# Optimization experiments

Hardware: AMD Instinct MI355X
Metric: run time of the kernel (lower is better)

Reference implementation:

```python
import jax, jax.numpy as jnp
import numpy as np

MKT_COEF = jnp.array([0.5, -1.0, 0.8, 0.6, 1.5, 0.4], dtype=jnp.float32)
RISK_COEF = jnp.array([0.5, -0.8, 0.6, 1.0, 1.2, 0.5], dtype=jnp.float32)
PI = 3.14159


def setup_inputs() -> dict:
    key = jax.random.key(0)
    k1, k2, k3, k4 = jax.random.split(key, 4)
    B, S, H, D = 128, 8192, 16, 6
    return {
        "sequence_embeddings": jax.random.normal(k1, (B, S, H), dtype=jnp.float32),
        "market_volatility": jax.random.uniform(k2, (B, S), dtype=jnp.float32),
        "risk_factors": jax.random.normal(k3, (B, S, D), dtype=jnp.float32),
        "router_w": jax.random.normal(k4, (D, H), dtype=jnp.float32) * 0.02,
        "router_b": jnp.zeros((D,), dtype=jnp.float32),
    }


def _expert_predictions(x, assignments):
    # x: (B,S,H); assignments: (B,S) int32
    mean = x.mean(-1, keepdims=True)                       # (B,S,1)
    std = jnp.std(x, axis=-1, keepdims=True, ddof=1)       # torch.std is unbiased
    d0 = jnp.tanh(x[:, :, :4].mean(-1, keepdims=True)) * (1.0 + std)
    d1 = jax.nn.sigmoid(mean) * 0.3 - 0.15
    d2 = x[:, :, :6].mean(-1, keepdims=True) * 0.8 + jnp.sin(x[:, :, 6:10].mean(-1, keepdims=True) * PI) * 0.4
    noise = jax.random.normal(jax.random.key(42), mean.shape, dtype=x.dtype) * 0.05
    d3 = jnp.tanh(x[:, :, :8].mean(-1, keepdims=True)) * 0.9 + noise
    d4 = jax.nn.relu(mean) ** 1.2 + std * 2.5 - 0.5
    d5 = jax.nn.sigmoid(mean) * 0.4 + jnp.tanh(std) * 0.2
    preds_all = jnp.concatenate([d0, d1, d2, d3, d4, d5], axis=-1)  # (B,S,6)
    return jnp.take_along_axis(preds_all, assignments[..., None].astype(jnp.int32), axis=-1)  # (B,S,1)


def reference(sequence_embeddings, market_volatility, risk_factors, router_w, router_b):
    x = sequence_embeddings
    logits = jnp.einsum("bsh,dh->bsd", x, router_w) + router_b            # (B,S,6)
    probs_base = jax.nn.softmax(logits, axis=-1)
    assignments = jnp.argmax(probs_base, axis=-1).astype(jnp.int32)       # (B,S)
    # training-mode market/risk adjusted straight-through probs
    adj = logits + market_volatility[..., None] * MKT_COEF * 0.3 + risk_factors * RISK_COEF * 0.3
    probs_diff = jax.nn.softmax(adj / 1.2, axis=-1)
    routing_probs = jax.lax.stop_gradient(probs_base) + probs_diff - jax.lax.stop_gradient(probs_diff)
    predictions = _expert_predictions(x, assignments)                     # (B,S,1)
    return predictions, routing_probs, assignments
```

## Files before the change

kernel.cpp:

```cpp
#include <hip/hip_runtime.h>
#include <math.h>

typedef float float4v __attribute__((ext_vector_type(4)));
typedef float float2v __attribute__((ext_vector_type(2)));

__device__ __forceinline__ unsigned rotl32(unsigned v, int n) {
  return (v << n) | (v >> (32 - n));
}

__device__ __forceinline__ float frcp(float x) { return __builtin_amdgcn_rcpf(x); }

__device__ __forceinline__ float ftanh(float x) {
  float t = __expf(2.0f * x);
  return 1.0f - 2.0f * frcp(t + 1.0f);
}

__device__ __forceinline__ float fsigmoid(float x) {
  return frcp(1.0f + __expf(-x));
}

__device__ __forceinline__ float jax_threefry_normal42_part(unsigned idx) {
  const unsigned ks0 = 0u;
  const unsigned ks1 = 42u;
  const unsigned ks2 = 0x1BD11BDAu ^ 42u;
  unsigned x0 = 0u + ks0;
  unsigned x1 = idx + ks1;
  const unsigned ks[3] = {ks0, ks1, ks2};
  const int rA[4] = {13, 15, 26, 6};
  const int rB[4] = {17, 29, 16, 24};
#pragma unroll
  for (int i = 0; i < 5; ++i) {
    const int* r = (i & 1) ? rB : rA;
#pragma unroll
    for (int k = 0; k < 4; ++k) {
      x0 += x1;
      x1 = rotl32(x1, r[k]);
      x1 ^= x0;
    }
    x0 += ks[(i + 1) % 3];
    x1 += ks[(i + 2) % 3] + (unsigned)(i + 1);
  }
  unsigned bits = x0 ^ x1;
  float u01 = __uint_as_float((bits >> 9) | 0x3f800000u) - 1.0f;
  const float lo = -0.99999994f;
  float u = fmaxf(lo, fmaf(u01, 2.0f, lo));
  float w = -__logf(1.0f - u * u);
  float p;
  if (w < 5.0f) {
    w = w - 2.5f;
    p = 2.81022636e-08f;
    p = fmaf(p, w, 3.43273939e-07f);
    p = fmaf(p, w, -3.5233877e-06f);
    p = fmaf(p, w, -4.39150654e-06f);
    p = fmaf(p, w, 0.00021858087f);
    p = fmaf(p, w, -0.00125372503f);
    p = fmaf(p, w, -0.00417768164f);
    p = fmaf(p, w, 0.246640727f);
    p = fmaf(p, w, 1.50140941f);
  } else {
    w = sqrtf(w) - 3.0f;
    p = -0.000200214257f;
    p = fmaf(p, w, 0.000100950558f);
    p = fmaf(p, w, 0.00134934322f);
    p = fmaf(p, w, -0.00367342844f);
    p = fmaf(p, w, 0.00573950773f);
    p = fmaf(p, w, -0.0076224613f);
    p = fmaf(p, w, 0.00943887047f);
    p = fmaf(p, w, 1.00167406f);
    p = fmaf(p, w, 2.83297682f);
  }
  return 1.41421354f * (p * u);
}

__global__ __launch_bounds__(256) void finance_moe_kernel(
    const float* __restrict__ emb,
    const float* __restrict__ rw,
    const float* __restrict__ rb,
    float* __restrict__ out,
    int ntok) {
  int t = blockIdx.x * blockDim.x + threadIdx.x;
  if (t >= ntok) return;

  const float4v* e4 = reinterpret_cast<const float4v*>(emb) + (size_t)t * 4;
  float4v a0 = e4[0];
  float4v a1 = e4[1];
  float4v a2 = e4[2];
  float4v a3 = e4[3];

  float noise = jax_threefry_normal42_part((unsigned)t) * 0.05f;

  float2v x2[8];
  x2[0] = a0.xy; x2[1] = a0.zw;
  x2[2] = a1.xy; x2[3] = a1.zw;
  x2[4] = a2.xy; x2[5] = a2.zw;
  x2[6] = a3.xy; x2[7] = a3.zw;
  float x[16];
  x[0] = a0.x; x[1] = a0.y; x[2] = a0.z; x[3] = a0.w;
  x[4] = a1.x; x[5] = a1.y; x[6] = a1.z; x[7] = a1.w;
  x[8] = a2.x; x[9] = a2.y; x[10] = a2.z; x[11] = a2.w;
  x[12] = a3.x; x[13] = a3.y; x[14] = a3.z; x[15] = a3.w;

  const float2v* rw2 = reinterpret_cast<const float2v*>(rw);
  float lg[6];
#pragma unroll
  for (int d = 0; d < 6; ++d) {
    float2v acc2; acc2.x = 0.0f; acc2.y = 0.0f;
#pragma unroll
    for (int p = 0; p < 8; ++p)
      acc2 = __builtin_elementwise_fma(x2[p], rw2[d * 8 + p], acc2);
    lg[d] = (acc2.x + acc2.y) + rb[d];
  }

  int a1i = 0, a2i = 0;
  float b1 = lg[0], b2 = -1e30f;
#pragma unroll
  for (int d = 1; d < 6; ++d) {
    if (lg[d] > b1) { b2 = b1; a2i = a1i; b1 = lg[d]; a1i = d; }
    else if (lg[d] > b2) { b2 = lg[d]; a2i = d; }
  }
  int amax = a1i;
  if (b1 - b2 < 2e-5f) {
    double A = 0.0, B = 0.0;
#pragma unroll
    for (int h = 0; h < 16; ++h) {
      A = fma((double)x[h], (double)rw[a1i * 16 + h], A);
      B = fma((double)x[h], (double)rw[a2i * 16 + h], B);
    }
    A += (double)rb[a1i];
    B += (double)rb[a2i];
    amax = (B > A || (B == A && a2i < a1i)) ? a2i : a1i;
  }

  float m = lg[0];
#pragma unroll
  for (int d = 1; d < 6; ++d) m = fmaxf(m, lg[d]);
  float eb[6], se = 0.0f;
#pragma unroll
  for (int d = 0; d < 6; ++d) { eb[d] = __expf(lg[d] - m); se += eb[d]; }
  float inv_se = frcp(se);
  float pb[6];
#pragma unroll
  for (int d = 0; d < 6; ++d) pb[d] = eb[d] * inv_se;

  float2v s2; s2.x = 0.0f; s2.y = 0.0f;
#pragma unroll
  for (int p = 0; p < 8; ++p) s2 = s2 + x2[p];
  float mean = (s2.x + s2.y) * (1.0f / 16.0f);
  float2v mean2; mean2.x = mean; mean2.y = mean;
  float2v ss2; ss2.x = 0.0f; ss2.y = 0.0f;
#pragma unroll
  for (int p = 0; p < 8; ++p) {
    float2v dv = x2[p] - mean2;
    ss2 = __builtin_elementwise_fma(dv, dv, ss2);
  }
  float stdv = sqrtf((ss2.x + ss2.y) * (1.0f / 15.0f));

  float s4 = ((x[0] + x[1]) + x[2]) + x[3];
  float s6 = ((((x[0] + x[1]) + x[2]) + x[3]) + x[4]) + x[5];
  float s610 = ((x[6] + x[7]) + x[8]) + x[9];
  float s8 = s6 + x[6] + x[7];

  float sig = fsigmoid(mean);
  float p0 = ftanh(s4 * 0.25f) * (1.0f + stdv);
  float p1 = sig * 0.3f - 0.15f;
  float p2 = (s6 * (1.0f / 6.0f)) * 0.8f + __sinf((s610 * 0.25f) * 3.14159f) * 0.4f;
  float p3 = ftanh(s8 * 0.125f) * 0.9f + noise;
  float r4 = fmaxf(mean, 0.0f);
  float p4 = __expf(1.2f * __logf(r4)) + stdv * 2.5f - 0.5f;
  float p5 = sig * 0.4f + ftanh(stdv) * 0.2f;

  float pred = (amax == 0) ? p0
             : (amax == 1) ? p1
             : (amax == 2) ? p2
             : (amax == 3) ? p3
             : (amax == 4) ? p4
                           : p5;

  out[t] = pred;
  float2v* po = reinterpret_cast<float2v*>(out + ntok) + (size_t)t * 3;
  float2v v0; v0.x = pb[0]; v0.y = pb[1];
  float2v v1; v1.x = pb[2]; v1.y = pb[3];
  float2v v2; v2.x = pb[4]; v2.y = pb[5];
  po[0] = v0;
  po[1] = v1;
  po[2] = v2;
  out[(size_t)ntok * 7 + t] = (float)amax;
}

extern "C" void kernel_launch(void* const* d_in, const int* in_sizes, int n_in,
                              void* d_out, int out_size, void* d_ws, size_t ws_size,
                              hipStream_t stream) {
  const float* emb = (const float*)d_in[0];
  const float* rw = (const float*)d_in[3];
  const float* rb = (const float*)d_in[4];
  float* out = (float*)d_out;
  int ntok = in_sizes[0] / 16;
  int block = 256;
  int grid = (ntok + block - 1) / block;
  hipLaunchKernelGGL(finance_moe_kernel, dim3(grid), dim3(block), 0, stream,
                     emb, rw, rb, out, ntok);
}
```

Baseline: 21.68 us.

## Stage embedding tile into LDS via direct global-to-LDS loads with swizzle

Full blocks now load their 256x16 embedding tile with global_load_lds, so each wave issues fully coalesced 16-byte-per-lane loads straight into shared memory, using an XOR swizzle to avoid bank conflicts on readback. The threefry noise computation is placed between the load issue and the barrier to hide latency. The aim is to replace strided per-thread 64-byte vector loads with coalesced transfers, at the cost of 16KB LDS per block, a barrier, and an extra LDS read pass.

```diff
diff --git a/kernel.cpp b/kernel.cpp
--- a/kernel.cpp
+++ b/kernel.cpp
@@ -72,33 +72,21 @@
   return 1.41421354f * (p * u);
 }
 
-__global__ __launch_bounds__(256) void finance_moe_kernel(
-    const float* __restrict__ emb,
-    const float* __restrict__ rw,
-    const float* __restrict__ rb,
-    float* __restrict__ out,
-    int ntok) {
-  int t = blockIdx.x * blockDim.x + threadIdx.x;
-  if (t >= ntok) return;
-
-  const float4v* e4 = reinterpret_cast<const float4v*>(emb) + (size_t)t * 4;
-  float4v a0 = e4[0];
-  float4v a1 = e4[1];
-  float4v a2 = e4[2];
-  float4v a3 = e4[3];
-
-  float noise = jax_threefry_normal42_part((unsigned)t) * 0.05f;
-
+__device__ __forceinline__ void token_body(
+    const float4v a[4], int t, float noise,
+    const float* __restrict__ rw, const float* __restrict__ rb,
+    float* __restrict__ out, int ntok) {
   float2v x2[8];
-  x2[0] = a0.xy; x2[1] = a0.zw;
-  x2[2] = a1.xy; x2[3] = a1.zw;
-  x2[4] = a2.xy; x2[5] = a2.zw;
-  x2[6] = a3.xy; x2[7] = a3.zw;
+  x2[0] = a[0].xy; x2[1] = a[0].zw;
+  x2[2] = a[1].xy; x2[3] = a[1].zw;
+  x2[4] = a[2].xy; x2[5] = a[2].zw;
+  x2[6] = a[3].xy; x2[7] = a[3].zw;
   float x[16];
-  x[0] = a0.x; x[1] = a0.y; x[2] = a0.z; x[3] = a0.w;
-  x[4] = a1.x; x[5] = a1.y; x[6] = a1.z; x[7] = a1.w;
-  x[8] = a2.x; x[9] = a2.y; x[10] = a2.z; x[11] = a2.w;
-  x[12] = a3.x; x[13] = a3.y; x[14] = a3.z; x[15] = a3.w;
+#pragma unroll
+  for (int q = 0; q < 4; ++q) {
+    x[q * 4 + 0] = a[q].x; x[q * 4 + 1] = a[q].y;
+    x[q * 4 + 2] = a[q].z; x[q * 4 + 3] = a[q].w;
+  }
 
   const float2v* rw2 = reinterpret_cast<const float2v*>(rw);
   float lg[6];
@@ -185,6 +173,59 @@
   po[1] = v1;
   po[2] = v2;
   out[(size_t)ntok * 7 + t] = (float)amax;
+}
+
+__global__ __launch_bounds__(256) void finance_moe_kernel(
+    const float* __restrict__ emb,
+    const float* __restrict__ rw,
+    const float* __restrict__ rb,
+    float* __restrict__ out,
+    int ntok) {
+  __shared__ float lds[256 * 16];
+
+  int tl = threadIdx.x;
+  int t = blockIdx.x * 256 + tl;
+  bool full = ((blockIdx.x + 1) * 256 <= ntok);
+
+  if (full) {
+    int lane = tl & 63;
+    int wave = tl >> 6;
+    const float* gbase = emb + (size_t)blockIdx.x * 256 * 16;
+#pragma unroll
+    for (int c = 0; c < 4; ++c) {
+      int chunk = wave * 4 + c;
+      int slot = chunk * 64 + lane;
+      int tok = slot >> 2;
+      int s = slot & 3;
+      int e = s ^ ((tok >> 1) & 3);
+      int gidx = tok * 4 + e;
+      const float* gp = gbase + (size_t)gidx * 4;
+      __builtin_amdgcn_global_load_lds(
+          (const __attribute__((address_space(1))) void*)gp,
+          (__attribute__((address_space(3))) void*)(lds + (size_t)chunk * 256),
+          16, 0, 0);
+    }
+
+    float noise = jax_threefry_normal42_part((unsigned)t) * 0.05f;
+
+    __syncthreads();
+
+    float4v a[4];
+#pragma unroll
+    for (int q = 0; q < 4; ++q) {
+      int s = q ^ ((tl >> 1) & 3);
+      a[q] = *reinterpret_cast<const float4v*>(&lds[tl * 16 + s * 4]);
+    }
+
+    token_body(a, t, noise, rw, rb, out, ntok);
+  } else {
+    if (t >= ntok) return;
+    const float4v* e4 = reinterpret_cast<const float4v*>(emb) + (size_t)t * 4;
+    float4v a[4];
+    a[0] = e4[0]; a[1] = e4[1]; a[2] = e4[2]; a[3] = e4[3];
+    float noise = jax_threefry_normal42_part((unsigned)t) * 0.05f;
+    token_body(a, t, noise, rw, rb, out, ntok);
+  }
 }
 
 extern "C" void kernel_launch(void* const* d_in, const int* in_sizes, int n_in,
```

Measured after the change: 21.86 us. No clear change (+0.8%).
